# Kernel tuning notes

Hardware: AMD Instinct MI355X
Metric: run time of the kernel (lower is better)

## Reference

```python
import jax, jax.numpy as jnp
import numpy as np

N, F, FH, H = 4096, 512, 64, 8  # nodes, in-features, per-head out-features, heads
ALPHA = 0.2  # LeakyReLU slope


def setup_inputs() -> dict:
    key = jax.random.key(0)
    ks = jax.random.split(key, 6)
    X = jax.random.normal(ks[0], (N, F), dtype=jnp.float32)
    A = (jax.random.uniform(ks[1], (N, N)) < 0.02).astype(jnp.float32)
    glorot_w = (2.0 / (F + FH)) ** 0.5
    glorot_a = (2.0 / (FH + 1)) ** 0.5
    W = jax.random.normal(ks[2], (H, F, FH), dtype=jnp.float32) * glorot_w
    a_self = jax.random.normal(ks[3], (H, FH), dtype=jnp.float32) * glorot_a
    a_neigh = jax.random.normal(ks[4], (H, FH), dtype=jnp.float32) * glorot_a
    b = jnp.zeros((H, FH), dtype=jnp.float32)
    return {"X": X, "A": A, "W": W, "a_self": a_self, "a_neigh": a_neigh, "b": b}


def reference(X, A, W, a_self, a_neigh, b):
    # per-head linear projection: [H, N, FH]
    feats = jnp.einsum('nf,hfo->hno', X, W)
    s_self = jnp.einsum('hno,ho->hn', feats, a_self)    # [H, N]
    s_neigh = jnp.einsum('hno,ho->hn', feats, a_neigh)  # [H, N]
    # additive logits: self_i + neigh_j -> [H, N, N]
    dense = s_self[:, :, None] + s_neigh[:, None, :]
    dense = jnp.where(dense > 0, dense, ALPHA * dense)  # LeakyReLU(0.2)
    dense = dense * A[None, :, :]                       # multiplicative adjacency (as in source)
    attn = jax.nn.softmax(dense, axis=-1)               # full-row softmax (as in source)
    # dropout is identity at inference
    out = jnp.einsum('hij,hjo->hio', attn, feats) + b[:, None, :]  # [H, N, FH]
    out = jnp.transpose(out, (1, 0, 2)).reshape(N, H * FH)         # concat heads
    return jax.nn.relu(out)
```

## Files before the change

kernel.cpp:

```cpp
#include <hip/hip_runtime.h>
#include <hip/hip_bf16.h>

#define N_NODES 4096
#define F_IN 512
#define FHD 64
#define H_HEADS 8
#define C_OUT 512
#define ALPHA 0.2f
#define MAXE 192

typedef __attribute__((ext_vector_type(8))) short bf16x8;
typedef __attribute__((ext_vector_type(4))) float f32x4;

static __device__ __forceinline__ unsigned short f2bf(float f) {
  __hip_bfloat16 h = __float2bfloat16(f);
  union { __hip_bfloat16 h; unsigned short u; } cvt;
  cvt.h = h;
  return cvt.u;
}

__global__ __launch_bounds__(256) void stream_kernel(
    const float* __restrict__ A, const float* __restrict__ X,
    const float* __restrict__ W, unsigned short* __restrict__ edges,
    int* __restrict__ degs, unsigned short* __restrict__ Xb,
    unsigned short* __restrict__ WbT, float* __restrict__ colsum) {
  __shared__ int wave_tot[4];
  __shared__ float sT[64][65];
  const int bid = blockIdx.x;
  const int tid = threadIdx.x;

  if (bid < N_NODES) {
    const int i = bid;
    const int wid = tid >> 6, lane = tid & 63;
    const float4* __restrict__ Arow4 =
        reinterpret_cast<const float4*>(A + (size_t)i * N_NODES);
    float4 v[4];
#pragma unroll
    for (int q = 0; q < 4; ++q) v[q] = Arow4[tid * 4 + q];
    int mask16 = 0;
#pragma unroll
    for (int q = 0; q < 4; ++q) {
      mask16 |= (v[q].x != 0.f) ? (1 << (q * 4 + 0)) : 0;
      mask16 |= (v[q].y != 0.f) ? (1 << (q * 4 + 1)) : 0;
      mask16 |= (v[q].z != 0.f) ? (1 << (q * 4 + 2)) : 0;
      mask16 |= (v[q].w != 0.f) ? (1 << (q * 4 + 3)) : 0;
    }
    int cnt = __popc(mask16);
    int inc = cnt;
#pragma unroll
    for (int s = 1; s < 64; s <<= 1) {
      int t = __shfl_up(inc, s, 64);
      if (lane >= s) inc += t;
    }
    if (lane == 63) wave_tot[wid] = inc;
    __syncthreads();
    int wprefix = 0, tot = 0;
#pragma unroll
    for (int w = 0; w < 4; ++w) {
      int t = wave_tot[w];
      if (w < wid) wprefix += t;
      tot += t;
    }
    int pos = wprefix + inc - cnt;
    const int jbase = tid * 16;
    unsigned short* __restrict__ erow = edges + (size_t)i * MAXE;
    while (mask16) {
      int k = __ffs(mask16) - 1;
      mask16 &= mask16 - 1;
      if (pos < MAXE) erow[pos] = (unsigned short)(jbase + k);
      ++pos;
    }
    if (tid == 0) degs[i] = tot < MAXE ? tot : MAXE;
  } else if (bid < N_NODES + 2048) {
    int idx = (bid - N_NODES) * 256 + tid;
    float4 v = reinterpret_cast<const float4*>(X)[idx];
    ushort4 u;
    u.x = f2bf(v.x); u.y = f2bf(v.y); u.z = f2bf(v.z); u.w = f2bf(v.w);
    reinterpret_cast<ushort4*>(Xb)[idx] = u;
  } else if (bid < N_NODES + 2048 + 64) {
    const int b2 = bid - (N_NODES + 2048);
    const int fblk = b2 & 7, h = b2 >> 3;
#pragma unroll
    for (int i = 0; i < 16; ++i) {
      int idx = tid + i * 256;
      int f = idx >> 6, o = idx & 63;
      sT[f][o] = W[((size_t)h * F_IN + fblk * 64 + f) * FHD + o];
    }
    __syncthreads();
#pragma unroll
    for (int i = 0; i < 16; ++i) {
      int idx = tid + i * 256;
      int o = idx >> 6, f = idx & 63;
      WbT[(size_t)h * FHD * F_IN + (size_t)o * F_IN + fblk * 64 + f] =
          f2bf(sT[f][o]);
    }
  } else {
    colsum[tid] = 0.f;
    colsum[tid + 256] = 0.f;
  }
}

__global__ __launch_bounds__(256) void gemm_feats_mfma_kernel(
    const unsigned short* __restrict__ Xb, const unsigned short* __restrict__ WbT,
    const float* __restrict__ a_self, const float* __restrict__ a_neigh,
    unsigned short* __restrict__ featsb,
    float* __restrict__ s_self, float* __restrict__ s_neigh,
    float* __restrict__ colsum) {
  const int h = blockIdx.y;
  const int n0 = blockIdx.x * 64;
  __shared__ unsigned short sX[2][64 * 72];
  __shared__ unsigned short sW[2][64 * 72];
  __shared__ float sred[4][64];
  const int tid = threadIdx.x;
  const int wid = tid >> 6, lane = tid & 63;
  const int l15 = lane & 15, l4 = lane >> 4;

  const int row = tid >> 2, seg = (tid & 3) * 16;
  const unsigned short* xsrc = Xb + (size_t)(n0 + row) * F_IN + seg;
  const unsigned short* wsrc = WbT + ((size_t)h * FHD + row) * F_IN + seg;
  const int soff = row * 72 + seg;

  f32x4 acc[4];
#pragma unroll
  for (int j = 0; j < 4; ++j) acc[j] = (f32x4){0.f, 0.f, 0.f, 0.f};

  *(bf16x8*)&sX[0][soff] = *(const bf16x8*)(xsrc);
  *(bf16x8*)&sX[0][soff + 8] = *(const bf16x8*)(xsrc + 8);
  *(bf16x8*)&sW[0][soff] = *(const bf16x8*)(wsrc);
  *(bf16x8*)&sW[0][soff + 8] = *(const bf16x8*)(wsrc + 8);
  __syncthreads();

  int cur = 0;
  for (int s = 0; s < 8; ++s) {
    bf16x8 px0, px1, pw0, pw1;
    const bool pf = (s < 7);
    if (pf) {
      const int k = (s + 1) * 64;
      px0 = *(const bf16x8*)(xsrc + k);
      px1 = *(const bf16x8*)(xsrc + k + 8);
      pw0 = *(const bf16x8*)(wsrc + k);
      pw1 = *(const bf16x8*)(wsrc + k + 8);
    }
#pragma unroll
    for (int kk = 0; kk < 2; ++kk) {
      bf16x8 a = *(const bf16x8*)&sX[cur][(wid * 16 + l15) * 72 + kk * 32 + l4 * 8];
#pragma unroll
      for (int tn = 0; tn < 4; ++tn) {
        bf16x8 b = *(const bf16x8*)&sW[cur][(tn * 16 + l15) * 72 + kk * 32 + l4 * 8];
        acc[tn] =
            __builtin_amdgcn_mfma_f32_16x16x32_bf16(a, b, acc[tn], 0, 0, 0);
      }
    }
    if (pf) {
      *(bf16x8*)&sX[cur ^ 1][soff] = px0;
      *(bf16x8*)&sX[cur ^ 1][soff + 8] = px1;
      *(bf16x8*)&sW[cur ^ 1][soff] = pw0;
      *(bf16x8*)&sW[cur ^ 1][soff + 8] = pw1;
      __syncthreads();
      cur ^= 1;
    }
  }

  float aS[4], aN[4];
#pragma unroll
  for (int tn = 0; tn < 4; ++tn) {
    aS[tn] = a_self[h * FHD + tn * 16 + l15];
    aN[tn] = a_neigh[h * FHD + tn * 16 + l15];
  }
#pragma unroll
  for (int r = 0; r < 4; ++r) {
    const int grow = n0 + wid * 16 + l4 * 4 + r;
#pragma unroll
    for (int tn = 0; tn < 4; ++tn)
      featsb[(size_t)grow * C_OUT + h * FHD + tn * 16 + l15] =
          f2bf(acc[tn][r]);
    float ps = 0.f, pn = 0.f;
#pragma unroll
    for (int tn = 0; tn < 4; ++tn) {
      float v = acc[tn][r];
      ps = fmaf(v, aS[tn], ps);
      pn = fmaf(v, aN[tn], pn);
    }
#pragma unroll
    for (int sh = 1; sh < 16; sh <<= 1) {
      ps += __shfl_xor(ps, sh, 64);
      pn += __shfl_xor(pn, sh, 64);
    }
    if (l15 == 0) {
      s_self[grow * 8 + h] = ps;
      s_neigh[grow * 8 + h] = pn;
    }
  }

  float psum[4];
#pragma unroll
  for (int tn = 0; tn < 4; ++tn) {
    float s = acc[tn][0] + acc[tn][1] + acc[tn][2] + acc[tn][3];
    s += __shfl_xor(s, 16, 64);
    s += __shfl_xor(s, 32, 64);
    psum[tn] = s;
  }
  if (l4 == 0) {
#pragma unroll
    for (int tn = 0; tn < 4; ++tn) sred[wid][tn * 16 + l15] = psum[tn];
  }
  __syncthreads();
  if (tid < 64) {
    float s = sred[0][tid] + sred[1][tid] + sred[2][tid] + sred[3][tid];
    atomicAdd(&colsum[h * FHD + tid], s);
  }
}

__global__ __launch_bounds__(256) void attn_kernel(
    const unsigned short* __restrict__ edges, const int* __restrict__ degs,
    const unsigned short* __restrict__ featsb,
    const float* __restrict__ s_self, const float* __restrict__ s_neigh,
    const float* __restrict__ colsum, const float* __restrict__ bias,
    float* __restrict__ out) {
  const int i = blockIdx.x;
  const int tid = threadIdx.x;
  const int wid = tid >> 6, lane = tid & 63;
  __shared__ int s_idx[MAXE];
  __shared__ uint2 s_iw[MAXE][8];
  __shared__ float sh_self[8];
  __shared__ float sh_e0[8], sh_invZ[8];
  __shared__ float s_part[128][4];

  const int deg = degs[i];
  if (tid < 8) sh_self[tid] = s_self[i * 8 + tid];
  if (tid < deg) s_idx[tid] = edges[(size_t)i * MAXE + tid];
  __syncthreads();

  for (int k = tid; k < deg * 8; k += 256) {
    int e = k >> 3, h = k & 7;
    int j = s_idx[e];
    float l = sh_self[h] + s_neigh[j * 8 + h];
    l = l > 0.f ? l : ALPHA * l;
    s_iw[e][h] = make_uint2((unsigned)(j << 10), __float_as_uint(l));
  }
  __syncthreads();

#pragma unroll
  for (int p = 0; p < 2; ++p) {
    const int h = wid * 2 + p;
    float m = -1e30f;
    for (int e = lane; e < deg; e += 64)
      m = fmaxf(m, __uint_as_float(s_iw[e][h].y));
#pragma unroll
    for (int s = 32; s > 0; s >>= 1) m = fmaxf(m, __shfl_xor(m, s, 64));
    m = fmaxf(m, 0.0f);
    float e0 = __expf(-m);
    float zs = 0.f;
    for (int e = lane; e < deg; e += 64) {
      float w = __expf(__uint_as_float(s_iw[e][h].y) - m);
      s_iw[e][h].y = __float_as_uint(w - e0);
      zs += w;
    }
#pragma unroll
    for (int s = 32; s > 0; s >>= 1) zs += __shfl_xor(zs, s, 64);
    if (lane == 0) {
      sh_e0[h] = e0;
      sh_invZ[h] = 1.0f / (zs + (float)(N_NODES - deg) * e0);
    }
  }
  __syncthreads();

  const int cq = tid & 127;
  const int half = tid >> 7;
  const int h = cq >> 4;
  const int dhalf = (deg + 1) >> 1;
  const int ebeg = half ? dhalf : 0;
  const int eend = half ? deg : dhalf;
  const char* __restrict__ fbase =
      reinterpret_cast<const char*>(featsb) + cq * 8;
  float a0 = 0.f, a1 = 0.f, a2 = 0.f, a3 = 0.f;
  float b0 = 0.f, b1 = 0.f, b2 = 0.f, b3 = 0.f;
  int e = ebeg;
  for (; e + 1 < eend; e += 2) {
    uint2 jw0 = s_iw[e][h];
    uint2 jw1 = s_iw[e + 1][h];
    float w0 = __uint_as_float(jw0.y);
    float w1 = __uint_as_float(jw1.y);
    uint2 u0 = *reinterpret_cast<const uint2*>(fbase + jw0.x);
    uint2 u1 = *reinterpret_cast<const uint2*>(fbase + jw1.x);
    a0 = fmaf(w0, __uint_as_float(u0.x << 16), a0);
    a1 = fmaf(w0, __uint_as_float(u0.x & 0xFFFF0000u), a1);
    a2 = fmaf(w0, __uint_as_float(u0.y << 16), a2);
    a3 = fmaf(w0, __uint_as_float(u0.y & 0xFFFF0000u), a3);
    b0 = fmaf(w1, __uint_as_float(u1.x << 16), b0);
    b1 = fmaf(w1, __uint_as_float(u1.x & 0xFFFF0000u), b1);
    b2 = fmaf(w1, __uint_as_float(u1.y << 16), b2);
    b3 = fmaf(w1, __uint_as_float(u1.y & 0xFFFF0000u), b3);
  }
  if (e < eend) {
    uint2 jw0 = s_iw[e][h];
    float w0 = __uint_as_float(jw0.y);
    uint2 u0 = *reinterpret_cast<const uint2*>(fbase + jw0.x);
    a0 = fmaf(w0, __uint_as_float(u0.x << 16), a0);
    a1 = fmaf(w0, __uint_as_float(u0.x & 0xFFFF0000u), a1);
    a2 = fmaf(w0, __uint_as_float(u0.y << 16), a2);
    a3 = fmaf(w0, __uint_as_float(u0.y & 0xFFFF0000u), a3);
  }
  a0 += b0; a1 += b1; a2 += b2; a3 += b3;
  if (half) {
    s_part[cq][0] = a0;
    s_part[cq][1] = a1;
    s_part[cq][2] = a2;
    s_part[cq][3] = a3;
  }
  __syncthreads();
  if (!half) {
    const float e0 = sh_e0[h], invZ = sh_invZ[h];
    const float4 cs = *reinterpret_cast<const float4*>(&colsum[cq * 4]);
    const float4 bb = *reinterpret_cast<const float4*>(&bias[cq * 4]);
    float v0 = (a0 + s_part[cq][0] + e0 * cs.x) * invZ + bb.x;
    float v1 = (a1 + s_part[cq][1] + e0 * cs.y) * invZ + bb.y;
    float v2 = (a2 + s_part[cq][2] + e0 * cs.z) * invZ + bb.z;
    float v3 = (a3 + s_part[cq][3] + e0 * cs.w) * invZ + bb.w;
    float4 o;
    o.x = v0 > 0.f ? v0 : 0.f;
    o.y = v1 > 0.f ? v1 : 0.f;
    o.z = v2 > 0.f ? v2 : 0.f;
    o.w = v3 > 0.f ? v3 : 0.f;
    *reinterpret_cast<float4*>(&out[(size_t)i * C_OUT + cq * 4]) = o;
  }
}

extern "C" void kernel_launch(void* const* d_in, const int* in_sizes, int n_in,
                              void* d_out, int out_size, void* d_ws, size_t ws_size,
                              hipStream_t stream) {
  const float* X = (const float*)d_in[0];
  const float* A = (const float*)d_in[1];
  const float* W = (const float*)d_in[2];
  const float* a_self = (const float*)d_in[3];
  const float* a_neigh = (const float*)d_in[4];
  const float* b = (const float*)d_in[5];
  float* out = (float*)d_out;

  char* ws = (char*)d_ws;
  unsigned short* featsb = (unsigned short*)ws;
  char* p = ws + (size_t)N_NODES * C_OUT * 2;
  float* s_self = (float*)p;  p += N_NODES * H_HEADS * 4;
  float* s_neigh = (float*)p; p += N_NODES * H_HEADS * 4;
  float* colsum = (float*)p;  p += C_OUT * 4;
  int* degs = (int*)p;        p += N_NODES * 4;
  unsigned short* edges = (unsigned short*)p;
  p += (size_t)N_NODES * MAXE * 2;
  unsigned short* WbT = (unsigned short*)p;

  unsigned short* Xb = (unsigned short*)d_out;

  stream_kernel<<<N_NODES + 2048 + 64 + 1, 256, 0, stream>>>(
      A, X, W, edges, degs, Xb, WbT, colsum);
  gemm_feats_mfma_kernel<<<dim3(64, 8), 256, 0, stream>>>(
      Xb, WbT, a_self, a_neigh, featsb, s_self, s_neigh, colsum);
  attn_kernel<<<N_NODES, 256, 0, stream>>>(edges, degs, featsb, s_self,
                                           s_neigh, colsum, b, out);
}
```

Baseline: 61.18 us.

## Overlap adjacency scan with feature GEMM and split attention shared arrays

```diff
diff --git a/kernel.cpp b/kernel.cpp
--- a/kernel.cpp
+++ b/kernel.cpp
@@ -8,6 +8,8 @@
 #define C_OUT 512
 #define ALPHA 0.2f
 #define MAXE 192
+#define MAXE_P 200
+#define GEMM_BLOCKS 512
 
 typedef __attribute__((ext_vector_type(8))) short bf16x8;
 typedef __attribute__((ext_vector_type(4))) float f32x4;
@@ -19,19 +21,60 @@
   return cvt.u;
 }
 
-__global__ __launch_bounds__(256) void stream_kernel(
-    const float* __restrict__ A, const float* __restrict__ X,
-    const float* __restrict__ W, unsigned short* __restrict__ edges,
-    int* __restrict__ degs, unsigned short* __restrict__ Xb,
-    unsigned short* __restrict__ WbT, float* __restrict__ colsum) {
-  __shared__ int wave_tot[4];
+__global__ __launch_bounds__(256) void conv_kernel(
+    const float* __restrict__ X, const float* __restrict__ W,
+    unsigned short* __restrict__ Xb, unsigned short* __restrict__ WbT,
+    float* __restrict__ colsum) {
   __shared__ float sT[64][65];
   const int bid = blockIdx.x;
   const int tid = threadIdx.x;
-
-  if (bid < N_NODES) {
-    const int i = bid;
-    const int wid = tid >> 6, lane = tid & 63;
+  if (bid < 2048) {
+    int idx = bid * 256 + tid;
+    float4 v = reinterpret_cast<const float4*>(X)[idx];
+    ushort4 u;
+    u.x = f2bf(v.x); u.y = f2bf(v.y); u.z = f2bf(v.z); u.w = f2bf(v.w);
+    reinterpret_cast<ushort4*>(Xb)[idx] = u;
+  } else if (bid < 2048 + 64) {
+    const int b2 = bid - 2048;
+    const int fblk = b2 & 7, h = b2 >> 3;
+#pragma unroll
+    for (int i = 0; i < 16; ++i) {
+      int idx = tid + i * 256;
+      int f = idx >> 6, o = idx & 63;
+      sT[f][o] = W[((size_t)h * F_IN + fblk * 64 + f) * FHD + o];
+    }
+    __syncthreads();
+#pragma unroll
+    for (int i = 0; i < 16; ++i) {
+      int idx = tid + i * 256;
+      int o = idx >> 6, f = idx & 63;
+      WbT[(size_t)h * FHD * F_IN + (size_t)o * F_IN + fblk * 64 + f] =
+          f2bf(sT[f][o]);
+    }
+  } else {
+    colsum[tid] = 0.f;
+    colsum[tid + 256] = 0.f;
+  }
+}
+
+__global__ __launch_bounds__(256) void gemm_scan_kernel(
+    const unsigned short* __restrict__ Xb, const unsigned short* __restrict__ WbT,
+    const float* __restrict__ a_self, const float* __restrict__ a_neigh,
+    const float* __restrict__ A,
+    unsigned short* __restrict__ featsb,
+    float* __restrict__ s_self, float* __restrict__ s_neigh,
+    float* __restrict__ colsum,
+    unsigned short* __restrict__ edges, int* __restrict__ degs) {
+  __shared__ unsigned short sX[2][64 * 72];
+  __shared__ unsigned short sW[2][64 * 72];
+  __shared__ float sred[4][64];
+  const int bid = blockIdx.x;
+  const int tid = threadIdx.x;
+  const int wid = tid >> 6, lane = tid & 63;
+
+  if (bid >= GEMM_BLOCKS) {
+    const int i = bid - GEMM_BLOCKS;
+    int* wave_tot = reinterpret_cast<int*>(&sred[0][0]);
     const float4* __restrict__ Arow4 =
         reinterpret_cast<const float4*>(A + (size_t)i * N_NODES);
     float4 v[4];
@@ -71,48 +114,11 @@
       ++pos;
     }
     if (tid == 0) degs[i] = tot < MAXE ? tot : MAXE;
-  } else if (bid < N_NODES + 2048) {
-    int idx = (bid - N_NODES) * 256 + tid;
-    float4 v = reinterpret_cast<const float4*>(X)[idx];
-    ushort4 u;
-    u.x = f2bf(v.x); u.y = f2bf(v.y); u.z = f2bf(v.z); u.w = f2bf(v.w);
-    reinterpret_cast<ushort4*>(Xb)[idx] = u;
-  } else if (bid < N_NODES + 2048 + 64) {
-    const int b2 = bid - (N_NODES + 2048);
-    const int fblk = b2 & 7, h = b2 >> 3;
-#pragma unroll
-    for (int i = 0; i < 16; ++i) {
-      int idx = tid + i * 256;
-      int f = idx >> 6, o = idx & 63;
-      sT[f][o] = W[((size_t)h * F_IN + fblk * 64 + f) * FHD + o];
-    }
-    __syncthreads();
-#pragma unroll
-    for (int i = 0; i < 16; ++i) {
-      int idx = tid + i * 256;
-      int o = idx >> 6, f = idx & 63;
-      WbT[(size_t)h * FHD * F_IN + (size_t)o * F_IN + fblk * 64 + f] =
-          f2bf(sT[f][o]);
-    }
-  } else {
-    colsum[tid] = 0.f;
-    colsum[tid + 256] = 0.f;
-  }
-}
-
-__global__ __launch_bounds__(256) void gemm_feats_mfma_kernel(
-    const unsigned short* __restrict__ Xb, const unsigned short* __restrict__ WbT,
-    const float* __restrict__ a_self, const float* __restrict__ a_neigh,
-    unsigned short* __restrict__ featsb,
-    float* __restrict__ s_self, float* __restrict__ s_neigh,
-    float* __restrict__ colsum) {
-  const int h = blockIdx.y;
-  const int n0 = blockIdx.x * 64;
-  __shared__ unsigned short sX[2][64 * 72];
-  __shared__ unsigned short sW[2][64 * 72];
-  __shared__ float sred[4][64];
-  const int tid = threadIdx.x;
-  const int wid = tid >> 6, lane = tid & 63;
+    return;
+  }
+
+  const int h = bid >> 6;
+  const int n0 = (bid & 63) * 64;
   const int l15 = lane & 15, l4 = lane >> 4;
 
   const int row = tid >> 2, seg = (tid & 3) * 16;
@@ -200,6 +206,7 @@
     s += __shfl_xor(s, 32, 64);
     psum[tn] = s;
   }
+  __syncthreads();
   if (l4 == 0) {
 #pragma unroll
     for (int tn = 0; tn < 4; ++tn) sred[wid][tn * 16 + l15] = psum[tn];
@@ -221,22 +228,26 @@
   const int tid = threadIdx.x;
   const int wid = tid >> 6, lane = tid & 63;
   __shared__ int s_idx[MAXE];
-  __shared__ uint2 s_iw[MAXE][8];
+  __shared__ int s_off[MAXE];
+  __shared__ float s_w[H_HEADS][MAXE_P];
   __shared__ float sh_self[8];
   __shared__ float sh_e0[8], sh_invZ[8];
   __shared__ float s_part[128][4];
 
   const int deg = degs[i];
   if (tid < 8) sh_self[tid] = s_self[i * 8 + tid];
-  if (tid < deg) s_idx[tid] = edges[(size_t)i * MAXE + tid];
+  if (tid < deg) {
+    int j = edges[(size_t)i * MAXE + tid];
+    s_idx[tid] = j;
+    s_off[tid] = j << 10;
+  }
   __syncthreads();
 
   for (int k = tid; k < deg * 8; k += 256) {
     int e = k >> 3, h = k & 7;
     int j = s_idx[e];
     float l = sh_self[h] + s_neigh[j * 8 + h];
-    l = l > 0.f ? l : ALPHA * l;
-    s_iw[e][h] = make_uint2((unsigned)(j << 10), __float_as_uint(l));
+    s_w[h][e] = l > 0.f ? l : ALPHA * l;
   }
   __syncthreads();
 
@@ -244,16 +255,15 @@
   for (int p = 0; p < 2; ++p) {
     const int h = wid * 2 + p;
     float m = -1e30f;
-    for (int e = lane; e < deg; e += 64)
-      m = fmaxf(m, __uint_as_float(s_iw[e][h].y));
+    for (int e = lane; e < deg; e += 64) m = fmaxf(m, s_w[h][e]);
 #pragma unroll
     for (int s = 32; s > 0; s >>= 1) m = fmaxf(m, __shfl_xor(m, s, 64));
     m = fmaxf(m, 0.0f);
     float e0 = __expf(-m);
     float zs = 0.f;
     for (int e = lane; e < deg; e += 64) {
-      float w = __expf(__uint_as_float(s_iw[e][h].y) - m);
-      s_iw[e][h].y = __float_as_uint(w - e0);
+      float w = __expf(s_w[h][e] - m);
+      s_w[h][e] = w - e0;
       zs += w;
     }
 #pragma unroll
@@ -277,12 +287,11 @@
   float b0 = 0.f, b1 = 0.f, b2 = 0.f, b3 = 0.f;
   int e = ebeg;
   for (; e + 1 < eend; e += 2) {
-    uint2 jw0 = s_iw[e][h];
-    uint2 jw1 = s_iw[e + 1][h];
-    float w0 = __uint_as_float(jw0.y);
-    float w1 = __uint_as_float(jw1.y);
-    uint2 u0 = *reinterpret_cast<const uint2*>(fbase + jw0.x);
-    uint2 u1 = *reinterpret_cast<const uint2*>(fbase + jw1.x);
+    float w0 = s_w[h][e];
+    float w1 = s_w[h][e + 1];
+    int o0 = s_off[e], o1 = s_off[e + 1];
+    uint2 u0 = *reinterpret_cast<const uint2*>(fbase + o0);
+    uint2 u1 = *reinterpret_cast<const uint2*>(fbase + o1);
     a0 = fmaf(w0, __uint_as_float(u0.x << 16), a0);
     a1 = fmaf(w0, __uint_as_float(u0.x & 0xFFFF0000u), a1);
     a2 = fmaf(w0, __uint_as_float(u0.y << 16), a2);
@@ -293,9 +302,8 @@
     b3 = fmaf(w1, __uint_as_float(u1.y & 0xFFFF0000u), b3);
   }
   if (e < eend) {
-    uint2 jw0 = s_iw[e][h];
-    float w0 = __uint_as_float(jw0.y);
-    uint2 u0 = *reinterpret_cast<const uint2*>(fbase + jw0.x);
+    float w0 = s_w[h][e];
+    uint2 u0 = *reinterpret_cast<const uint2*>(fbase + s_off[e]);
     a0 = fmaf(w0, __uint_as_float(u0.x << 16), a0);
     a1 = fmaf(w0, __uint_as_float(u0.x & 0xFFFF0000u), a1);
     a2 = fmaf(w0, __uint_as_float(u0.y << 16), a2);
@@ -350,10 +358,10 @@
 
   unsigned short* Xb = (unsigned short*)d_out;
 
-  stream_kernel<<<N_NODES + 2048 + 64 + 1, 256, 0, stream>>>(
-      A, X, W, edges, degs, Xb, WbT, colsum);
-  gemm_feats_mfma_kernel<<<dim3(64, 8), 256, 0, stream>>>(
-      Xb, WbT, a_self, a_neigh, featsb, s_self, s_neigh, colsum);
+  conv_kernel<<<2048 + 64 + 1, 256, 0, stream>>>(X, W, Xb, WbT, colsum);
+  gemm_scan_kernel<<<GEMM_BLOCKS + N_NODES, 256, 0, stream>>>(
+      Xb, WbT, a_self, a_neigh, A, featsb, s_self, s_neigh, colsum, edges,
+      degs);
   attn_kernel<<<N_NODES, 256, 0, stream>>>(edges, degs, featsb, s_self,
                                            s_neigh, colsum, b, out);
 }
```

Result: faster. 57.77 us (-5.6%).
